# Performance work log

Measured on AMD Instinct MI355X. Metric: run time of the kernel, lower is better.

## Reference

```python
import jax, jax.numpy as jnp
import numpy as np

NUMSTEPS = 10  # message-passing rounds (SeqGGNN numsteps)

def setup_inputs() -> dict:
    key = jax.random.key(0)
    ks = jax.random.split(key, 10)
    B, S, H, V = 64, 512, 256, 32000
    s = 0.05  # keep activations in a stable range
    return {
        "x": jax.random.randint(ks[0], (B, S), 0, V),
        "emb": jax.random.normal(ks[1], (V, H), jnp.float32) * s,
        "W_edge": jax.random.normal(ks[2], (3, H, H), jnp.float32) * s,  # [fwd, bwd, self]
        "b_edge": jax.random.normal(ks[3], (3, H), jnp.float32) * s,
        "W_ih": jax.random.normal(ks[4], (3 * H, H), jnp.float32) * s,
        "W_hh": jax.random.normal(ks[5], (3 * H, H), jnp.float32) * s,
        "b_ih": jax.random.normal(ks[6], (3 * H,), jnp.float32) * s,
        "b_hh": jax.random.normal(ks[7], (3 * H,), jnp.float32) * s,
        "out_w": jax.random.normal(ks[8], (V, H), jnp.float32) * s,
        "out_b": jax.random.normal(ks[9], (V,), jnp.float32) * s,
    }

def _gru(m, h, W_ih, W_hh, b_ih, b_hh):
    # torch.nn.GRUCell semantics with input m, state h
    gi = m @ W_ih.T + b_ih
    gh = h @ W_hh.T + b_hh
    i_r, i_z, i_n = jnp.split(gi, 3, axis=-1)
    h_r, h_z, h_n = jnp.split(gh, 3, axis=-1)
    r = jax.nn.sigmoid(i_r + h_r)
    z = jax.nn.sigmoid(i_z + h_z)
    n = jnp.tanh(i_n + r * h_n)
    return (1.0 - z) * n + z * h

def reference(x, emb, W_edge, b_edge, W_ih, W_hh, b_ih, b_hh, out_w, out_b):
    # x: [B,S] int ids; chain graph per row with 3 edge types:
    #   fwd:  j -> j+1 (node j+1 receives W_edge[0] h_j + b_edge[0])
    #   bwd:  j+1 -> j (node j receives W_edge[1] h_{j+1} + b_edge[1])
    #   self: j -> j   (W_edge[2] h_j + b_edge[2])
    h0 = emb[x]  # [B,S,H]

    def step(h, _):
        t_fwd = jnp.einsum('bsh,hk->bsk', h, W_edge[0]) + b_edge[0]
        t_bwd = jnp.einsum('bsh,hk->bsk', h, W_edge[1]) + b_edge[1]
        m_self = jnp.einsum('bsh,hk->bsk', h, W_edge[2]) + b_edge[2]
        # scatter-sum along the chain == shift with zero pad at boundaries
        m_fwd = jnp.pad(t_fwd[:, :-1], ((0, 0), (1, 0), (0, 0)))
        m_bwd = jnp.pad(t_bwd[:, 1:], ((0, 0), (0, 1), (0, 0)))
        m = m_fwd + m_bwd + m_self
        h_new = _gru(m, h, W_ih, W_hh, b_ih, b_hh)
        return h_new, None

    h, _ = jax.lax.scan(step, h0, None, length=NUMSTEPS)
    last = h[:, -1, :]  # [B,H]
    return last @ out_w.T + out_b  # [B,V]
```

## Files before the change

### kernel.cpp

```cpp
#include <hip/hip_runtime.h>
#include <math.h>

#define Bb 64
#define Ss 512
#define Hh 256
#define Vv 32000
#define BS (Bb*Ss)
#define NSTEPS 10

typedef __attribute__((ext_vector_type(8))) short bf16x8;
typedef __attribute__((ext_vector_type(4))) float f32x4;
typedef unsigned short u16;

#define MFMA(a,b,c) __builtin_amdgcn_mfma_f32_16x16x32_bf16((a),(b),(c),0,0,0)

__device__ __forceinline__ u16 f2bf(float f) {
    unsigned u = __float_as_uint(f);
    u += 0x7fffu + ((u >> 16) & 1u);
    return (u16)(u >> 16);
}
__device__ __forceinline__ float bf2f(u16 h) {
    return __uint_as_float(((unsigned)h) << 16);
}
__device__ __forceinline__ int nmap(int j, int g) {
    return ((j >> 4) << 6) | (g << 4) | (j & 15);
}
#define GLL(src, dst) __builtin_amdgcn_global_load_lds( \
    (const __attribute__((address_space(1))) void*)(src), \
    (__attribute__((address_space(3))) void*)(dst), 16, 0, 0)

__global__ __launch_bounds__(256)
void k_prep_big(const float* __restrict__ We, const float* __restrict__ Wih,
                const float* __restrict__ Whh, u16* __restrict__ Bbig) {
    __shared__ u16 Aps[64 * 32];
    __shared__ u16 Bps[64 * 32];
    const int p = blockIdx.y, seg = p / 3, g = p % 3;
    const int segmap0 = (seg == 0) ? 2 : (seg == 1 ? 0 : 1);
    const float* Wseg = We + segmap0 * 65536;
    const int kt = (blockIdx.x >> 2) * 64, jt = (blockIdx.x & 3) * 64;
    const int t = threadIdx.x;
    const int lane = t & 63, wid = t >> 6;
    const int wy = (wid >> 1) * 32, wx = (wid & 1) * 32;
    const int lr = lane & 15, hi = lane >> 4;

    f32x4 acc[2][2];
    #pragma unroll
    for (int a = 0; a < 2; ++a)
        #pragma unroll
        for (int b = 0; b < 2; ++b) acc[a][b] = 0.0f;

    for (int ks = 0; ks < 8; ++ks) {
        const int k0 = ks * 32;
        {
            int r = t >> 2, kc = t & 3;
            const float* sa = Wseg + (kt + r) * 256 + k0 + kc * 8;
            float4 a0 = *(const float4*)sa, a1 = *(const float4*)(sa + 4);
            bf16x8 va;
            va[0]=(short)f2bf(a0.x); va[1]=(short)f2bf(a0.y); va[2]=(short)f2bf(a0.z); va[3]=(short)f2bf(a0.w);
            va[4]=(short)f2bf(a1.x); va[5]=(short)f2bf(a1.y); va[6]=(short)f2bf(a1.z); va[7]=(short)f2bf(a1.w);
            ((bf16x8*)Aps)[r * 4 + (kc ^ (r & 3))] = va;
            const float* sb = Wih + (g * 256 + jt + r) * 256 + k0 + kc * 8;
            float4 b0 = *(const float4*)sb, b1 = *(const float4*)(sb + 4);
            bf16x8 vb;
            vb[0]=(short)f2bf(b0.x); vb[1]=(short)f2bf(b0.y); vb[2]=(short)f2bf(b0.z); vb[3]=(short)f2bf(b0.w);
            vb[4]=(short)f2bf(b1.x); vb[5]=(short)f2bf(b1.y); vb[6]=(short)f2bf(b1.z); vb[7]=(short)f2bf(b1.w);
            ((bf16x8*)Bps)[r * 4 + (kc ^ (r & 3))] = vb;
        }
        __syncthreads();
        bf16x8 af[2], bfv[2];
        #pragma unroll
        for (int f = 0; f < 2; ++f) {
            int ra = wy + f * 16 + lr;
            af[f]  = ((const bf16x8*)Aps)[ra * 4 + (hi ^ (ra & 3))];
            int rb = wx + f * 16 + lr;
            bfv[f] = ((const bf16x8*)Bps)[rb * 4 + (hi ^ (rb & 3))];
        }
        #pragma unroll
        for (int fm = 0; fm < 2; ++fm)
            #pragma unroll
            for (int fn = 0; fn < 2; ++fn)
                acc[fm][fn] = MFMA(af[fm], bfv[fn], acc[fm][fn]);
        __syncthreads();
    }
    #pragma unroll
    for (int fm = 0; fm < 2; ++fm)
        #pragma unroll
        for (int fn = 0; fn < 2; ++fn) {
            int kbase = kt + wy + fm * 16 + hi * 4;
            int j     = jt + wx + fn * 16 + lr;
            float4 wv = make_float4(0.f, 0.f, 0.f, 0.f);
            if (seg == 0 && g < 2)
                wv = *(const float4*)(Whh + (g * 256 + j) * 256 + kbase);
            ushort4 o;
            o.x = f2bf(acc[fm][fn][0] + wv.x);
            o.y = f2bf(acc[fm][fn][1] + wv.y);
            o.z = f2bf(acc[fm][fn][2] + wv.z);
            o.w = f2bf(acc[fm][fn][3] + wv.w);
            *(ushort4*)(Bbig + (size_t)nmap(j, g) * 768 + seg * 256 + kbase) = o;
        }
}

__global__ __launch_bounds__(256)
void k_prep_hn(const float* __restrict__ Whh, u16* __restrict__ Bbig) {
    int j = blockIdx.x / 3;
    int k = (blockIdx.x % 3) * 256 + threadIdx.x;
    Bbig[(size_t)nmap(j, 3) * 768 + k] =
        (k < 256) ? f2bf(Whh[(512 + j) * 256 + k]) : (u16)0;
}

__global__ __launch_bounds__(256)
void k_prep_bias(const float* __restrict__ Wih, const float* __restrict__ b_edge,
                 const float* __restrict__ b_ih, const float* __restrict__ b_hh,
                 float* __restrict__ bias) {
    int id = blockIdx.x * 256 + threadIdx.x;
    int c = id >> 10, n = id & 1023;
    int g = (n >> 4) & 3;
    int j = ((n >> 6) << 4) | (n & 15);
    float a;
    if (g == 3) {
        a = b_hh[512 + j];
    } else {
        a = b_ih[g * 256 + j] + (g < 2 ? b_hh[g * 256 + j] : 0.f);
        const float* wrow = Wih + (g * 256 + j) * 256;
        for (int k = 0; k < 256; ++k) {
            float eb = b_edge[512 + k] + (c != 0 ? b_edge[k] : 0.f)
                     + (c != 2 ? b_edge[256 + k] : 0.f);
            a += eb * wrow[k];
        }
    }
    bias[c * 1024 + n] = a;
}

__global__ __launch_bounds__(256)
void k_embed(const int* __restrict__ x, const float* __restrict__ emb,
             u16* __restrict__ h) {
    int idx = blockIdx.x * 256 + threadIdx.x;
    int row = idx >> 5, c8 = idx & 31;
    long long tok = x[row];
    const float4* e = reinterpret_cast<const float4*>(emb + tok * Hh + c8 * 8);
    float4 a = e[0], b = e[1];
    bf16x8 v;
    v[0]=(short)f2bf(a.x); v[1]=(short)f2bf(a.y); v[2]=(short)f2bf(a.z); v[3]=(short)f2bf(a.w);
    v[4]=(short)f2bf(b.x); v[5]=(short)f2bf(b.y); v[6]=(short)f2bf(b.z); v[7]=(short)f2bf(b.w);
    ((bf16x8*)h)[idx] = v;
}

__global__ __launch_bounds__(512, 2)
void k_step(const u16* __restrict__ hin, const u16* __restrict__ Bbig,
            const float* __restrict__ bias, u16* __restrict__ hout) {
    __shared__ __attribute__((aligned(16))) u16 As[2][256 * 64 + 512];
    __shared__ __attribute__((aligned(16))) u16 Bs[2][2][128 * 64];
    const int t = threadIdx.x;
    const int lane = t & 63, wid = t >> 6;
    const int swz = (blockIdx.x & 7) * 64 + (blockIdx.x >> 3);
    const int rowBlk = (swz >> 2) * 256;
    const int colBlk = (swz & 3) * 256;
    const int wy = wid >> 2, wx = wid & 3;
    const int lr = lane & 15, hi = lane >> 4;
    const int s0 = rowBlk & (Ss - 1);

    const int q   = t >> 3;
    const int off = ((t & 7) ^ (q & 7)) << 3;

    const u16* pA[4];
    const u16* pB[4];
    #pragma unroll
    for (int j = 0; j < 4; ++j) {
        pA[j] = hin  + (size_t)(rowBlk + j * 64 + q) * Hh  + off;
        pB[j] = Bbig + (size_t)(colBlk + j * 64 + q) * 768 + off;
    }
    const u16* haloSrc = hin
        + (size_t)(s0 == 0 ? rowBlk + 256 : rowBlk - 1) * Hh + lane * 8;

    f32x4 acc[8][4];
    #pragma unroll
    for (int a = 0; a < 8; ++a)
        #pragma unroll
        for (int b = 0; b < 4; ++b) acc[a][b] = 0.0f;

    auto STAGE_A = [&](int kqn) {
        u16* aD = (u16*)As[kqn & 1];
        const int o = kqn * 64;
        #pragma unroll
        for (int h = 0; h < 2; ++h)
            #pragma unroll
            for (int i = 0; i < 2; ++i)
                GLL(pA[h * 2 + i] + o, aD + h * 8192 + (i * 512 + wid * 64) * 8);
        if (wid == 0) GLL(haloSrc + o, aD + 16384);
    };
    auto STAGE_B = [&](int itn) {
        const int kqn = itn / 3, segn = itn % 3;
        u16* bD = (u16*)Bs[itn & 1];
        const int o = segn * 256 + kqn * 64;
        #pragma unroll
        for (int h = 0; h < 2; ++h)
            #pragma unroll
            for (int i = 0; i < 2; ++i)
                GLL(pB[h * 2 + i] + o, bD + h * 8192 + (i * 512 + wid * 64) * 8);
    };
    auto COMPUTE = [&](int kq, int seg) {
        const bf16x8* aB = (const bf16x8*)As[kq & 1];
        const bf16x8* bB = (const bf16x8*)Bs[(kq * 3 + seg) & 1];
        const int d = (seg == 0) ? 0 : (seg == 1 ? -1 : 1);
        #pragma unroll
        for (int kk = 0; kk < 2; ++kk) {
            bf16x8 bfv[4];
            #pragma unroll
            for (int f = 0; f < 4; ++f) {
                if (seg != 0 && f == 3) continue;
                int rwb = (wx & 1) * 64 + f * 16 + lr;
                bfv[f] = bB[(wx >> 1) * 1024 + rwb * 8 + ((kk * 4 + hi) ^ (lr & 7))];
            }
            #pragma unroll
            for (int mh = 0; mh < 2; ++mh) {
                bf16x8 af[4];
                #pragma unroll
                for (int f = 0; f < 4; ++f) {
                    int rr  = wy * 128 + mh * 64 + f * 16 + lr + d;
                    int idx = rr * 8 + ((kk * 4 + hi) ^ (rr & 7));
                    bf16x8 av;
                    if (d < 0 && mh == 0 && f == 0) {
                        bool bd = (wy == 0) && (lr == 0);
                        av = aB[bd ? (2048 + kk * 4 + hi) : idx];
                        if (bd && s0 == 0) { bf16x8 zz = 0; av = zz; }
                    } else if (d > 0 && mh == 1 && f == 3) {
                        bool bd = (wy == 1) && (lr == 15);
                        av = aB[idx];
                        if (bd && s0 != 0) { bf16x8 zz = 0; av = zz; }
                    } else {
                        av = aB[idx];
                    }
                    af[f] = av;
                }
                __builtin_amdgcn_s_setprio(1);
                #pragma unroll
                for (int fm = 0; fm < 4; ++fm)
                    #pragma unroll
                    for (int fn = 0; fn < 4; ++fn)
                        if (seg == 0 || fn < 3)
                            acc[mh * 4 + fm][fn] =
                                MFMA(af[fm], bfv[fn], acc[mh * 4 + fm][fn]);
                __builtin_amdgcn_s_setprio(0);
            }
        }
    };

    STAGE_A(0);
    STAGE_B(0);
    __syncthreads();
    #pragma unroll
    for (int kq = 0; kq < 4; ++kq)
        #pragma unroll
        for (int seg = 0; seg < 3; ++seg) {
            const int it = kq * 3 + seg;
            if (it < 11) STAGE_B(it + 1);
            if (seg == 0 && kq < 3) STAGE_A(kq + 1);
            COMPUTE(kq, seg);
            __syncthreads();
        }

    const int hq = (colBlk >> 2) + wx * 16;
    #pragma unroll
    for (int mf = 0; mf < 8; ++mf)
        #pragma unroll
        for (int i = 0; i < 4; ++i) {
            int row = rowBlk + wy * 128 + mf * 16 + hi * 4 + i;
            int s = row & (Ss - 1);
            int cls = (s == 0) ? 0 : ((s == Ss - 1) ? 2 : 1);
            const float* bp = bias + cls * 1024 + colBlk + wx * 64 + lr;
            float vr = acc[mf][0][i] + bp[0];
            float vz = acc[mf][1][i] + bp[16];
            float vn = acc[mf][2][i] + bp[32];
            float vh = acc[mf][3][i] + bp[48];
            float r = 1.f / (1.f + __expf(-vr));
            float z = 1.f / (1.f + __expf(-vz));
            float e = __expf(2.f * (vn + r * vh));
            float n = 1.f - 2.f / (e + 1.f);
            int hcol = hq + lr;
            float hold = bf2f(hin[(size_t)row * Hh + hcol]);
            hout[(size_t)row * Hh + hcol] = f2bf(n + z * (hold - n));
        }
}

__global__ __launch_bounds__(256)
void k_out(const u16* __restrict__ h, const float* __restrict__ out_w,
           const float* __restrict__ out_b, float* __restrict__ out) {
    __shared__ u16 As[64 * 256];
    const int t = threadIdx.x;
    const int lane = t & 63, wid = t >> 6;
    const int colBlk = blockIdx.x * 128;
    const int wc = wid * 32;
    const int lr = lane & 15, hi = lane >> 4;

    #pragma unroll
    for (int i = 0; i < 8; ++i) {
        int c = t + i * 256;
        int r = c >> 5, kc = c & 31;
        bf16x8 v = *(const bf16x8*)(h + ((size_t)(r * Ss + (Ss - 1))) * Hh + kc * 8);
        ((bf16x8*)As)[r * 32 + (kc ^ (r & 7))] = v;
    }
    __syncthreads();

    f32x4 acc[4][2];
    #pragma unroll
    for (int a = 0; a < 4; ++a) { acc[a][0] = 0.0f; acc[a][1] = 0.0f; }

    #pragma unroll
    for (int ks = 0; ks < 8; ++ks) {
        bf16x8 af[4];
        #pragma unroll
        for (int f = 0; f < 4; ++f) {
            int ra = f * 16 + lr;
            af[f] = ((const bf16x8*)As)[ra * 32 + ((ks * 4 + hi) ^ (ra & 7))];
        }
        #pragma unroll
        for (int fn = 0; fn < 2; ++fn) {
            int n = colBlk + wc + fn * 16 + lr;
            const float* wp = out_w + (size_t)n * 256 + ks * 32 + hi * 8;
            float4 w0 = *(const float4*)wp, w1 = *(const float4*)(wp + 4);
            bf16x8 vb;
            vb[0]=(short)f2bf(w0.x); vb[1]=(short)f2bf(w0.y); vb[2]=(short)f2bf(w0.z); vb[3]=(short)f2bf(w0.w);
            vb[4]=(short)f2bf(w1.x); vb[5]=(short)f2bf(w1.y); vb[6]=(short)f2bf(w1.z); vb[7]=(short)f2bf(w1.w);
            #pragma unroll
            for (int fm = 0; fm < 4; ++fm)
                acc[fm][fn] = MFMA(af[fm], vb, acc[fm][fn]);
        }
    }
    #pragma unroll
    for (int fm = 0; fm < 4; ++fm)
        #pragma unroll
        for (int fn = 0; fn < 2; ++fn)
            #pragma unroll
            for (int i = 0; i < 4; ++i) {
                int row = fm * 16 + hi * 4 + i;
                int col = colBlk + wc + fn * 16 + lr;
                out[(size_t)row * Vv + col] = acc[fm][fn][i] + out_b[col];
            }
}

extern "C" void kernel_launch(void* const* d_in, const int* in_sizes, int n_in,
                              void* d_out, int out_size, void* d_ws, size_t ws_size,
                              hipStream_t stream) {
    const int*   x      = (const int*)  d_in[0];
    const float* emb    = (const float*)d_in[1];
    const float* W_edge = (const float*)d_in[2];
    const float* b_edge = (const float*)d_in[3];
    const float* W_ih   = (const float*)d_in[4];
    const float* W_hh   = (const float*)d_in[5];
    const float* b_ih   = (const float*)d_in[6];
    const float* b_hh   = (const float*)d_in[7];
    const float* out_w  = (const float*)d_in[8];
    const float* out_b  = (const float*)d_in[9];
    float* out = (float*)d_out;

    u16* hA   = (u16*)d_ws;
    u16* hB   = hA + (size_t)BS * Hh;
    u16* Bbig = hB + (size_t)BS * Hh;
    float* bias = (float*)(Bbig + (size_t)1024 * 768);

    k_prep_big <<<dim3(16, 9), 256, 0, stream>>>(W_edge, W_ih, W_hh, Bbig);
    k_prep_hn  <<<768, 256, 0, stream>>>(W_hh, Bbig);
    k_prep_bias<<<12, 256, 0, stream>>>(W_ih, b_edge, b_ih, b_hh, bias);
    k_embed    <<<BS * Hh / 8 / 256, 256, 0, stream>>>(x, emb, hA);

    u16* cur = hA;
    u16* nxt = hB;
    for (int step = 0; step < NSTEPS; ++step) {
        k_step<<<512, 512, 0, stream>>>(cur, Bbig, bias, nxt);
        u16* tmp = cur; cur = nxt; nxt = tmp;
    }
    k_out<<<Vv / 128, 256, 0, stream>>>(cur, out_w, out_b, out);
}
```

Measured before the change: 543.4 us.

## Halve step-kernel row tile and drop LDS double buffering for higher occupancy

```diff
diff --git a/kernel.cpp b/kernel.cpp
--- a/kernel.cpp
+++ b/kernel.cpp
@@ -145,15 +145,15 @@
     ((bf16x8*)h)[idx] = v;
 }
 
-__global__ __launch_bounds__(512, 2)
+__global__ __launch_bounds__(512, 4)
 void k_step(const u16* __restrict__ hin, const u16* __restrict__ Bbig,
             const float* __restrict__ bias, u16* __restrict__ hout) {
-    __shared__ __attribute__((aligned(16))) u16 As[2][256 * 64 + 512];
-    __shared__ __attribute__((aligned(16))) u16 Bs[2][2][128 * 64];
+    __shared__ __attribute__((aligned(16))) u16 As[1152 * 8];
+    __shared__ __attribute__((aligned(16))) u16 Bs[256 * 64];
     const int t = threadIdx.x;
     const int lane = t & 63, wid = t >> 6;
-    const int swz = (blockIdx.x & 7) * 64 + (blockIdx.x >> 3);
-    const int rowBlk = (swz >> 2) * 256;
+    const int swz = (blockIdx.x & 7) * 128 + (blockIdx.x >> 3);
+    const int rowBlk = (swz >> 2) * 128;
     const int colBlk = (swz & 3) * 256;
     const int wy = wid >> 2, wx = wid & 3;
     const int lr = lane & 15, hi = lane >> 4;
@@ -162,73 +162,69 @@
     const int q   = t >> 3;
     const int off = ((t & 7) ^ (q & 7)) << 3;
 
-    const u16* pA[4];
+    const u16* pA[2];
+    pA[0] = hin + (size_t)(rowBlk + q) * Hh + off;
+    pA[1] = hin + (size_t)(rowBlk + 64 + q) * Hh + off;
     const u16* pB[4];
     #pragma unroll
-    for (int j = 0; j < 4; ++j) {
-        pA[j] = hin  + (size_t)(rowBlk + j * 64 + q) * Hh  + off;
+    for (int j = 0; j < 4; ++j)
         pB[j] = Bbig + (size_t)(colBlk + j * 64 + q) * 768 + off;
-    }
-    const u16* haloSrc = hin
-        + (size_t)(s0 == 0 ? rowBlk + 256 : rowBlk - 1) * Hh + lane * 8;
-
-    f32x4 acc[8][4];
-    #pragma unroll
-    for (int a = 0; a < 8; ++a)
+    const int haloLoRow = (s0 > 0)          ? rowBlk - 1   : rowBlk;
+    const int haloHiRow = (s0 < Ss - 128)   ? rowBlk + 128 : rowBlk;
+    const u16* haloLo = hin + (size_t)haloLoRow * Hh + lane * 8;
+    const u16* haloHi = hin + (size_t)haloHiRow * Hh + lane * 8;
+
+    f32x4 acc[4][4];
+    #pragma unroll
+    for (int a = 0; a < 4; ++a)
         #pragma unroll
         for (int b = 0; b < 4; ++b) acc[a][b] = 0.0f;
 
-    auto STAGE_A = [&](int kqn) {
-        u16* aD = (u16*)As[kqn & 1];
-        const int o = kqn * 64;
-        #pragma unroll
-        for (int h = 0; h < 2; ++h)
+    #pragma unroll
+    for (int kq = 0; kq < 4; ++kq) {
+        const int ko = kq * 64;
+        GLL(pA[0] + ko, As + (size_t)(wid * 64) * 8);
+        GLL(pA[1] + ko, As + (size_t)(512 + wid * 64) * 8);
+        if (wid == 0) GLL(haloLo + ko, As + 1024 * 8);
+        if (wid == 1) GLL(haloHi + ko, As + 1088 * 8);
+
+        #pragma unroll
+        for (int seg = 0; seg < 3; ++seg) {
+            const int o = seg * 256 + ko;
+            if (seg == 0 || wid < 6) {
+                #pragma unroll
+                for (int j = 0; j < 4; ++j)
+                    GLL(pB[j] + o, Bs + (size_t)(j * 512 + wid * 64) * 8);
+            }
+            __syncthreads();
+            const int d = (seg == 0) ? 0 : (seg == 1 ? -1 : 1);
             #pragma unroll
-            for (int i = 0; i < 2; ++i)
-                GLL(pA[h * 2 + i] + o, aD + h * 8192 + (i * 512 + wid * 64) * 8);
-        if (wid == 0) GLL(haloSrc + o, aD + 16384);
-    };
-    auto STAGE_B = [&](int itn) {
-        const int kqn = itn / 3, segn = itn % 3;
-        u16* bD = (u16*)Bs[itn & 1];
-        const int o = segn * 256 + kqn * 64;
-        #pragma unroll
-        for (int h = 0; h < 2; ++h)
-            #pragma unroll
-            for (int i = 0; i < 2; ++i)
-                GLL(pB[h * 2 + i] + o, bD + h * 8192 + (i * 512 + wid * 64) * 8);
-    };
-    auto COMPUTE = [&](int kq, int seg) {
-        const bf16x8* aB = (const bf16x8*)As[kq & 1];
-        const bf16x8* bB = (const bf16x8*)Bs[(kq * 3 + seg) & 1];
-        const int d = (seg == 0) ? 0 : (seg == 1 ? -1 : 1);
-        #pragma unroll
-        for (int kk = 0; kk < 2; ++kk) {
-            bf16x8 bfv[4];
-            #pragma unroll
-            for (int f = 0; f < 4; ++f) {
-                if (seg != 0 && f == 3) continue;
-                int rwb = (wx & 1) * 64 + f * 16 + lr;
-                bfv[f] = bB[(wx >> 1) * 1024 + rwb * 8 + ((kk * 4 + hi) ^ (lr & 7))];
-            }
-            #pragma unroll
-            for (int mh = 0; mh < 2; ++mh) {
+            for (int kk = 0; kk < 2; ++kk) {
+                const int kc = kk * 4 + hi;
+                bf16x8 bfv[4];
+                #pragma unroll
+                for (int f = 0; f < 4; ++f) {
+                    if (seg != 0 && f == 3) continue;
+                    int rb = wx * 64 + f * 16 + lr;
+                    bfv[f] = ((const bf16x8*)Bs)[rb * 8 + (kc ^ (rb & 7))];
+                }
                 bf16x8 af[4];
                 #pragma unroll
                 for (int f = 0; f < 4; ++f) {
-                    int rr  = wy * 128 + mh * 64 + f * 16 + lr + d;
-                    int idx = rr * 8 + ((kk * 4 + hi) ^ (rr & 7));
+                    int rr = wy * 64 + f * 16 + lr + d;
                     bf16x8 av;
-                    if (d < 0 && mh == 0 && f == 0) {
-                        bool bd = (wy == 0) && (lr == 0);
-                        av = aB[bd ? (2048 + kk * 4 + hi) : idx];
+                    if (d < 0 && wy == 0 && f == 0) {
+                        bool bd = (lr == 0);
+                        int idx = bd ? (1024 + kc) : (rr * 8 + (kc ^ (rr & 7)));
+                        av = ((const bf16x8*)As)[idx];
                         if (bd && s0 == 0) { bf16x8 zz = 0; av = zz; }
-                    } else if (d > 0 && mh == 1 && f == 3) {
-                        bool bd = (wy == 1) && (lr == 15);
-                        av = aB[idx];
-                        if (bd && s0 != 0) { bf16x8 zz = 0; av = zz; }
+                    } else if (d > 0 && wy == 1 && f == 3) {
+                        bool bd = (lr == 15);
+                        int idx = bd ? (1088 + kc) : (rr * 8 + (kc ^ (rr & 7)));
+                        av = ((const bf16x8*)As)[idx];
+                        if (bd && s0 == Ss - 128) { bf16x8 zz = 0; av = zz; }
                     } else {
-                        av = aB[idx];
+                        av = ((const bf16x8*)As)[rr * 8 + (kc ^ (rr & 7))];
                     }
                     af[f] = av;
                 }
@@ -238,33 +234,19 @@
                     #pragma unroll
                     for (int fn = 0; fn < 4; ++fn)
                         if (seg == 0 || fn < 3)
-                            acc[mh * 4 + fm][fn] =
-                                MFMA(af[fm], bfv[fn], acc[mh * 4 + fm][fn]);
+                            acc[fm][fn] = MFMA(af[fm], bfv[fn], acc[fm][fn]);
                 __builtin_amdgcn_s_setprio(0);
             }
-        }
-    };
-
-    STAGE_A(0);
-    STAGE_B(0);
-    __syncthreads();
-    #pragma unroll
-    for (int kq = 0; kq < 4; ++kq)
-        #pragma unroll
-        for (int seg = 0; seg < 3; ++seg) {
-            const int it = kq * 3 + seg;
-            if (it < 11) STAGE_B(it + 1);
-            if (seg == 0 && kq < 3) STAGE_A(kq + 1);
-            COMPUTE(kq, seg);
             __syncthreads();
         }
+    }
 
     const int hq = (colBlk >> 2) + wx * 16;
     #pragma unroll
-    for (int mf = 0; mf < 8; ++mf)
+    for (int mf = 0; mf < 4; ++mf)
         #pragma unroll
         for (int i = 0; i < 4; ++i) {
-            int row = rowBlk + wy * 128 + mf * 16 + hi * 4 + i;
+            int row = rowBlk + wy * 64 + mf * 16 + hi * 4 + i;
             int s = row & (Ss - 1);
             int cls = (s == 0) ? 0 : ((s == Ss - 1) ? 2 : 1);
             const float* bp = bias + cls * 1024 + colBlk + wx * 64 + lr;
@@ -366,7 +348,7 @@
     u16* cur = hA;
     u16* nxt = hB;
     for (int step = 0; step < NSTEPS; ++step) {
-        k_step<<<512, 512, 0, stream>>>(cur, Bbig, bias, nxt);
+        k_step<<<1024, 512, 0, stream>>>(cur, Bbig, bias, nxt);
         u16* tmp = cur; cur = nxt; nxt = tmp;
     }
     k_out<<<Vv / 128, 256, 0, stream>>>(cur, out_w, out_b, out);
```

Result: slower. 1.136 ms (+109.1%).
